# Optimization experiments

Measured on AMD Instinct MI355X. Metric: run time of the kernel, lower is better.

Reference implementation:

```python
import jax, jax.numpy as jnp
import numpy as np

C = 256


def setup_inputs() -> dict:
    key = jax.random.key(0)
    keys = jax.random.split(key, 14)
    shp = (2, C, 64, 256)
    inp = {f"x{i}": jax.random.normal(keys[i], shp, dtype=jnp.float32) for i in range(12)}
    # ConvTranspose2d weight [in, out, 1, 1] -> squeezed to [in, out]
    inp["W"] = jax.random.normal(keys[12], (C, C), dtype=jnp.float32) * 0.05
    inp["b"] = jax.random.normal(keys[13], (C,), dtype=jnp.float32) * 0.05
    return inp


def reference(x0, x1, x2, x3, x4, x5, x6, x7, x8, x9, x10, x11, W, b):
    xs = jnp.stack([x0, x1, x2, x3, x4, x5, x6, x7, x8, x9, x10, x11])  # [12,B,C,H,Wd]
    # 1x1 conv-transpose == per-pixel matmul over channels (weight is [in,out])
    y = jnp.einsum('ibchw,co->ibohw', xs, W)  # [12,B,C,H,Wd]
    n, B, Co, H, Wd = y.shape
    Hout = 12 * H
    # interleave: output row 12*h + i comes from tensor i, row h
    out = jnp.transpose(y, (1, 2, 3, 0, 4)).reshape(B, Co, Hout, Wd)
    # bias multiplicity: conv-transpose bias fills ALL rows of each (12H-11)-row
    # intermediate; padded copy j covers rows j .. j+12H-12 of the final buffer
    r = jnp.arange(Hout)
    count = (jnp.minimum(11, r) - jnp.maximum(0, r - Hout + 12) + 1).astype(out.dtype)
    out = out + b[:, None, None] * count[None, :, None]
    return out
```

## Files before the change

### kernel.cpp

```cpp
#include <hip/hip_runtime.h>


typedef __attribute__((ext_vector_type(8))) short bf16x8;
typedef __attribute__((ext_vector_type(4))) float f32x4;

#define ROW_B 512
#define TILE_B (64 * ROW_B)

struct Ptrs12 { const float* p[12]; };

__device__ __forceinline__ unsigned f2bf1(float f) {
  unsigned u = __float_as_uint(f);
  return (u + 0x7FFFu + ((u >> 16) & 1u)) >> 16;
}

__global__ void w_prepass(const float* __restrict__ W, unsigned short* __restrict__ Wf) {
  int idx = blockIdx.x * 256 + threadIdx.x;
  int j = idx & 7, l = (idx >> 3) & 63, s = (idx >> 9) & 7, u = idx >> 12;
  int c = s * 32 + (l >> 4) * 8 + j;
  int o = u * 16 + (l & 15);
  Wf[idx] = (unsigned short)f2bf1(W[c * 256 + o]);
}

__global__ __launch_bounds__(512, 2) void gemm12(Ptrs12 xs,
                                                 const unsigned short* __restrict__ Wf,
                                                 const float* __restrict__ bias,
                                                 float* __restrict__ out) {
  __shared__ char smem[2 * TILE_B];
  const int tid = threadIdx.x;
  const int v = tid >> 6;
  const int l = tid & 63;
  const int q = l >> 4;
  const int m = l & 15;

  bf16x8 wf[2][8];
#pragma unroll
  for (int tt = 0; tt < 2; ++tt)
#pragma unroll
    for (int s = 0; s < 8; ++s) {
      int u = v * 2 + tt;
      wf[tt][s] = *(const bf16x8*)(Wf + (((u * 8 + s) * 64 + l) << 3));
    }
  const float bv0 = bias[v * 32 + m];
  const float bv1 = bias[v * 32 + 16 + m];

  const int tile0 = blockIdx.x * 12;
  float4 pf[2][4];

  auto tload = [&](int tile) {
    int row = tile >> 2, w0 = (tile & 3) << 6;
    int i = row >> 7, bb = (row >> 6) & 1, h = row & 63;
    const float* xp = xs.p[i] + (size_t)bb * 4194304 + h * 256 + w0 + m * 4;
#pragma unroll
    for (int it = 0; it < 2; ++it) {
      int cb = it * 128 + v * 16 + q * 4;
#pragma unroll
      for (int dc = 0; dc < 4; ++dc)
        pf[it][dc] = *(const float4*)(xp + (size_t)(cb + dc) * 16384);
    }
  };
  auto twrite = [&](int bs) {
    char* lb = smem + bs * TILE_B;
#pragma unroll
    for (int it = 0; it < 2; ++it) {
      int cb = it * 128 + v * 16 + q * 4;
#pragma unroll
      for (int k = 0; k < 4; ++k) {
        unsigned lo = f2bf1(((const float*)&pf[it][0])[k]) |
                      (f2bf1(((const float*)&pf[it][1])[k]) << 16);
        unsigned hi = f2bf1(((const float*)&pf[it][2])[k]) |
                      (f2bf1(((const float*)&pf[it][3])[k]) << 16);
        uint2 val; val.x = lo; val.y = hi;
        *(uint2*)(lb + (m * 4 + k) * ROW_B + cb * 2) = val;
      }
    }
  };

  tload(tile0);
  twrite(0);
  __syncthreads();

#pragma unroll 1
  for (int mt = 0; mt < 12; ++mt) {
    int tile = tile0 + mt;
    if (mt < 11) tload(tile + 1);

    f32x4 acc[4][2];
#pragma unroll
    for (int a = 0; a < 4; ++a) { acc[a][0] = 0.0f; acc[a][1] = 0.0f; }

    const char* lb = smem + (mt & 1) * TILE_B;
#pragma unroll
    for (int s = 0; s < 8; ++s) {
      bf16x8 af[4];
#pragma unroll
      for (int m16 = 0; m16 < 4; ++m16)
        af[m16] = *(const bf16x8*)(lb + (m16 * 16 + m) * ROW_B + s * 64 + q * 16);
#pragma unroll
      for (int m16 = 0; m16 < 4; ++m16) {
        acc[m16][0] = __builtin_amdgcn_mfma_f32_16x16x32_bf16(af[m16], wf[0][s], acc[m16][0], 0, 0, 0);
        acc[m16][1] = __builtin_amdgcn_mfma_f32_16x16x32_bf16(af[m16], wf[1][s], acc[m16][1], 0, 0, 0);
      }
    }

    if (mt < 11) twrite((mt + 1) & 1);

    int row = tile >> 2, w0 = (tile & 3) << 6;
    int i = row >> 7, bb = (row >> 6) & 1, h = row & 63;
    int r = h * 12 + i;
    int cnt_i = (r < 11 ? r : 11) - (r > 756 ? r - 756 : 0) + 1;
    float cnt = (float)cnt_i;
    size_t ob = (size_t)bb * 50331648u + (size_t)r * 256 + w0 + q * 4;
#pragma unroll
    for (int tt = 0; tt < 2; ++tt) {
      float ba = (tt ? bv1 : bv0) * cnt;
      float* op = out + ob + (size_t)(v * 32 + tt * 16 + m) * 196608;
#pragma unroll
      for (int m16 = 0; m16 < 4; ++m16) {
        float4 sv;
        sv.x = acc[m16][tt][0] + ba;
        sv.y = acc[m16][tt][1] + ba;
        sv.z = acc[m16][tt][2] + ba;
        sv.w = acc[m16][tt][3] + ba;
        *(float4*)(op + m16 * 16) = sv;
      }
    }
    __syncthreads();
  }
}

extern "C" void kernel_launch(void* const* d_in, const int* in_sizes, int n_in,
                              void* d_out, int out_size, void* d_ws, size_t ws_size,
                              hipStream_t stream) {
  Ptrs12 xs;
  for (int i = 0; i < 12; ++i) xs.p[i] = (const float*)d_in[i];
  const float* W = (const float*)d_in[12];
  const float* bias = (const float*)d_in[13];
  unsigned short* Wf = (unsigned short*)d_ws;

  hipLaunchKernelGGL(w_prepass, dim3(256), dim3(256), 0, stream, W, Wf);
  hipLaunchKernelGGL(gemm12, dim3(512), dim3(512), 0, stream, xs, Wf, bias, (float*)d_out);
}
```

Before: 710.5 us.

## Use 1024-thread blocks with 16 output channels per wave and swizzled LDS

Result: slower. 778.2 us (+9.5%).

```diff
diff --git a/kernel.cpp b/kernel.cpp
--- a/kernel.cpp
+++ b/kernel.cpp
@@ -22,10 +22,17 @@
   Wf[idx] = (unsigned short)f2bf1(W[c * 256 + o]);
 }
 
-__global__ __launch_bounds__(512, 2) void gemm12(Ptrs12 xs,
-                                                 const unsigned short* __restrict__ Wf,
-                                                 const float* __restrict__ bias,
-                                                 float* __restrict__ out) {
+#define LBAR() do {                                   \
+  __builtin_amdgcn_sched_barrier(0);                  \
+  asm volatile("s_waitcnt lgkmcnt(0)" ::: "memory");  \
+  __builtin_amdgcn_s_barrier();                       \
+  __builtin_amdgcn_sched_barrier(0);                  \
+} while (0)
+
+__global__ __launch_bounds__(1024, 4) void gemm12(Ptrs12 xs,
+                                                  const unsigned short* __restrict__ Wf,
+                                                  const float* __restrict__ bias,
+                                                  float* __restrict__ out) {
   __shared__ char smem[2 * TILE_B];
   const int tid = threadIdx.x;
   const int v = tid >> 6;
@@ -33,99 +40,92 @@
   const int q = l >> 4;
   const int m = l & 15;
 
-  bf16x8 wf[2][8];
+  bf16x8 wf[8];
 #pragma unroll
-  for (int tt = 0; tt < 2; ++tt)
-#pragma unroll
-    for (int s = 0; s < 8; ++s) {
-      int u = v * 2 + tt;
-      wf[tt][s] = *(const bf16x8*)(Wf + (((u * 8 + s) * 64 + l) << 3));
-    }
-  const float bv0 = bias[v * 32 + m];
-  const float bv1 = bias[v * 32 + 16 + m];
+  for (int s = 0; s < 8; ++s)
+    wf[s] = *(const bf16x8*)(Wf + (((v * 8 + s) * 64 + l) << 3));
+  const float bv = bias[v * 16 + m];
 
-  const int tile0 = blockIdx.x * 12;
-  float4 pf[2][4];
+  const int tile0 = blockIdx.x * 24;
+  float4 pf[4];
 
   auto tload = [&](int tile) {
     int row = tile >> 2, w0 = (tile & 3) << 6;
     int i = row >> 7, bb = (row >> 6) & 1, h = row & 63;
     const float* xp = xs.p[i] + (size_t)bb * 4194304 + h * 256 + w0 + m * 4;
+    int cb = v * 16 + q * 4;
 #pragma unroll
-    for (int it = 0; it < 2; ++it) {
-      int cb = it * 128 + v * 16 + q * 4;
-#pragma unroll
-      for (int dc = 0; dc < 4; ++dc)
-        pf[it][dc] = *(const float4*)(xp + (size_t)(cb + dc) * 16384);
-    }
+    for (int dc = 0; dc < 4; ++dc)
+      pf[dc] = *(const float4*)(xp + (size_t)(cb + dc) * 16384);
   };
   auto twrite = [&](int bs) {
     char* lb = smem + bs * TILE_B;
+    const int col = v * 32 + q * 8;
 #pragma unroll
-    for (int it = 0; it < 2; ++it) {
-      int cb = it * 128 + v * 16 + q * 4;
-#pragma unroll
-      for (int k = 0; k < 4; ++k) {
-        unsigned lo = f2bf1(((const float*)&pf[it][0])[k]) |
-                      (f2bf1(((const float*)&pf[it][1])[k]) << 16);
-        unsigned hi = f2bf1(((const float*)&pf[it][2])[k]) |
-                      (f2bf1(((const float*)&pf[it][3])[k]) << 16);
-        uint2 val; val.x = lo; val.y = hi;
-        *(uint2*)(lb + (m * 4 + k) * ROW_B + cb * 2) = val;
-      }
+    for (int k = 0; k < 4; ++k) {
+      unsigned lo = f2bf1(((const float*)&pf[0])[k]) |
+                    (f2bf1(((const float*)&pf[1])[k]) << 16);
+      unsigned hi = f2bf1(((const float*)&pf[2])[k]) |
+                    (f2bf1(((const float*)&pf[3])[k]) << 16);
+      uint2 val; val.x = lo; val.y = hi;
+      int row = m * 4 + k;
+      unsigned a = (unsigned)(row * ROW_B + col) ^ ((unsigned)(row & 7) << 4);
+      *(uint2*)(lb + a) = val;
     }
   };
 
   tload(tile0);
   twrite(0);
-  __syncthreads();
+  LBAR();
 
 #pragma unroll 1
-  for (int mt = 0; mt < 12; ++mt) {
-    int tile = tile0 + mt;
-    if (mt < 11) tload(tile + 1);
+  for (int mt = 0; mt < 24; ++mt) {
+    const int tile = tile0 + mt;
+    if (mt < 23) tload(tile + 1);
 
-    f32x4 acc[4][2];
+    f32x4 acc[4];
 #pragma unroll
-    for (int a = 0; a < 4; ++a) { acc[a][0] = 0.0f; acc[a][1] = 0.0f; }
+    for (int z = 0; z < 4; ++z) acc[z] = 0.0f;
 
     const char* lb = smem + (mt & 1) * TILE_B;
 #pragma unroll
     for (int s = 0; s < 8; ++s) {
       bf16x8 af[4];
 #pragma unroll
+      for (int m16 = 0; m16 < 4; ++m16) {
+        int row = m16 * 16 + m;
+        unsigned a = (unsigned)(row * ROW_B + s * 64 + q * 16) ^
+                     ((unsigned)(row & 7) << 4);
+        af[m16] = *(const bf16x8*)(lb + a);
+      }
+#pragma unroll
       for (int m16 = 0; m16 < 4; ++m16)
-        af[m16] = *(const bf16x8*)(lb + (m16 * 16 + m) * ROW_B + s * 64 + q * 16);
+        acc[m16] = __builtin_amdgcn_mfma_f32_16x16x32_bf16(af[m16], wf[s], acc[m16], 0, 0, 0);
+    }
+
+    {
+      int row = tile >> 2, w0 = (tile & 3) << 6;
+      int i = row >> 7, bb = (row >> 6) & 1, h = row & 63;
+      int r = h * 12 + i;
+      int cnt_i = (r < 11 ? r : 11) - (r > 756 ? r - 756 : 0) + 1;
+      float ba = bv * (float)cnt_i;
+      float* op = out + (size_t)bb * 50331648u + (size_t)r * 256 + w0 + q * 4
+                      + (size_t)(v * 16 + m) * 196608;
 #pragma unroll
       for (int m16 = 0; m16 < 4; ++m16) {
-        acc[m16][0] = __builtin_amdgcn_mfma_f32_16x16x32_bf16(af[m16], wf[0][s], acc[m16][0], 0, 0, 0);
-        acc[m16][1] = __builtin_amdgcn_mfma_f32_16x16x32_bf16(af[m16], wf[1][s], acc[m16][1], 0, 0, 0);
+        float4 sv;
+        sv.x = acc[m16][0] + ba;
+        sv.y = acc[m16][1] + ba;
+        sv.z = acc[m16][2] + ba;
+        sv.w = acc[m16][3] + ba;
+        *(float4*)(op + m16 * 16) = sv;
       }
     }
 
-    if (mt < 11) twrite((mt + 1) & 1);
-
-    int row = tile >> 2, w0 = (tile & 3) << 6;
-    int i = row >> 7, bb = (row >> 6) & 1, h = row & 63;
-    int r = h * 12 + i;
-    int cnt_i = (r < 11 ? r : 11) - (r > 756 ? r - 756 : 0) + 1;
-    float cnt = (float)cnt_i;
-    size_t ob = (size_t)bb * 50331648u + (size_t)r * 256 + w0 + q * 4;
-#pragma unroll
-    for (int tt = 0; tt < 2; ++tt) {
-      float ba = (tt ? bv1 : bv0) * cnt;
-      float* op = out + ob + (size_t)(v * 32 + tt * 16 + m) * 196608;
-#pragma unroll
-      for (int m16 = 0; m16 < 4; ++m16) {
-        float4 sv;
-        sv.x = acc[m16][tt][0] + ba;
-        sv.y = acc[m16][tt][1] + ba;
-        sv.z = acc[m16][tt][2] + ba;
-        sv.w = acc[m16][tt][3] + ba;
-        *(float4*)(op + m16 * 16) = sv;
-      }
+    if (mt < 23) {
+      twrite((mt + 1) & 1);
+      LBAR();
     }
-    __syncthreads();
   }
 }
 
@@ -139,5 +139,5 @@
   unsigned short* Wf = (unsigned short*)d_ws;
 
   hipLaunchKernelGGL(w_prepass, dim3(256), dim3(256), 0, stream, W, Wf);
-  hipLaunchKernelGGL(gemm12, dim3(512), dim3(512), 0, stream, xs, Wf, bias, (float*)d_out);
+  hipLaunchKernelGGL(gemm12, dim3(256), dim3(1024), 0, stream, xs, Wf, bias, (float*)d_out);
 }
```

## Halve tile width, raise occupancy, swizzle LDS, and use a lighter barrier

Applied to the files above, without the earlier changes.

Result: slower. 803.9 us (+13.1%).

```diff
diff --git a/kernel.cpp b/kernel.cpp
--- a/kernel.cpp
+++ b/kernel.cpp
@@ -5,7 +5,7 @@
 typedef __attribute__((ext_vector_type(4))) float f32x4;
 
 #define ROW_B 512
-#define TILE_B (64 * ROW_B)
+#define TILE_B (32 * ROW_B)
 
 struct Ptrs12 { const float* p[12]; };
 
@@ -22,7 +22,14 @@
   Wf[idx] = (unsigned short)f2bf1(W[c * 256 + o]);
 }
 
-__global__ __launch_bounds__(512, 2) void gemm12(Ptrs12 xs,
+#define LBAR() do {                                   \
+  __builtin_amdgcn_sched_barrier(0);                  \
+  asm volatile("s_waitcnt lgkmcnt(0)" ::: "memory");  \
+  __builtin_amdgcn_s_barrier();                       \
+  __builtin_amdgcn_sched_barrier(0);                  \
+} while (0)
+
+__global__ __launch_bounds__(512, 4) void gemm12(Ptrs12 xs,
                                                  const unsigned short* __restrict__ Wf,
                                                  const float* __restrict__ bias,
                                                  float* __restrict__ out) {
@@ -44,88 +51,92 @@
   const float bv0 = bias[v * 32 + m];
   const float bv1 = bias[v * 32 + 16 + m];
 
-  const int tile0 = blockIdx.x * 12;
-  float4 pf[2][4];
+  const int wg = m & 7;
+  const int chb = v * 32 + q * 8 + ((m >> 3) << 2);
+
+  const int tile0 = blockIdx.x * 24;
+  float4 pf[4];
 
   auto tload = [&](int tile) {
-    int row = tile >> 2, w0 = (tile & 3) << 6;
+    int row = tile >> 3, w0 = (tile & 7) << 5;
     int i = row >> 7, bb = (row >> 6) & 1, h = row & 63;
-    const float* xp = xs.p[i] + (size_t)bb * 4194304 + h * 256 + w0 + m * 4;
+    const float* xp = xs.p[i] + (size_t)bb * 4194304 + h * 256 + w0 + wg * 4;
 #pragma unroll
-    for (int it = 0; it < 2; ++it) {
-      int cb = it * 128 + v * 16 + q * 4;
-#pragma unroll
-      for (int dc = 0; dc < 4; ++dc)
-        pf[it][dc] = *(const float4*)(xp + (size_t)(cb + dc) * 16384);
-    }
+    for (int dc = 0; dc < 4; ++dc)
+      pf[dc] = *(const float4*)(xp + (size_t)(chb + dc) * 16384);
   };
   auto twrite = [&](int bs) {
     char* lb = smem + bs * TILE_B;
 #pragma unroll
-    for (int it = 0; it < 2; ++it) {
-      int cb = it * 128 + v * 16 + q * 4;
-#pragma unroll
-      for (int k = 0; k < 4; ++k) {
-        unsigned lo = f2bf1(((const float*)&pf[it][0])[k]) |
-                      (f2bf1(((const float*)&pf[it][1])[k]) << 16);
-        unsigned hi = f2bf1(((const float*)&pf[it][2])[k]) |
-                      (f2bf1(((const float*)&pf[it][3])[k]) << 16);
-        uint2 val; val.x = lo; val.y = hi;
-        *(uint2*)(lb + (m * 4 + k) * ROW_B + cb * 2) = val;
-      }
+    for (int k = 0; k < 4; ++k) {
+      unsigned lo = f2bf1(((const float*)&pf[0])[k]) |
+                    (f2bf1(((const float*)&pf[1])[k]) << 16);
+      unsigned hi = f2bf1(((const float*)&pf[2])[k]) |
+                    (f2bf1(((const float*)&pf[3])[k]) << 16);
+      uint2 val; val.x = lo; val.y = hi;
+      int row = wg * 4 + k;
+      unsigned a = (unsigned)(row * ROW_B + chb * 2) ^ ((unsigned)(row & 7) << 4);
+      *(uint2*)(lb + a) = val;
     }
   };
 
   tload(tile0);
   twrite(0);
-  __syncthreads();
+  LBAR();
 
 #pragma unroll 1
-  for (int mt = 0; mt < 12; ++mt) {
-    int tile = tile0 + mt;
-    if (mt < 11) tload(tile + 1);
+  for (int mt = 0; mt < 24; ++mt) {
+    const int tile = tile0 + mt;
+    if (mt < 23) tload(tile + 1);
 
-    f32x4 acc[4][2];
+    f32x4 acc[2][2];
 #pragma unroll
-    for (int a = 0; a < 4; ++a) { acc[a][0] = 0.0f; acc[a][1] = 0.0f; }
+    for (int z = 0; z < 2; ++z) { acc[z][0] = 0.0f; acc[z][1] = 0.0f; }
 
     const char* lb = smem + (mt & 1) * TILE_B;
 #pragma unroll
     for (int s = 0; s < 8; ++s) {
-      bf16x8 af[4];
+      bf16x8 af[2];
 #pragma unroll
-      for (int m16 = 0; m16 < 4; ++m16)
-        af[m16] = *(const bf16x8*)(lb + (m16 * 16 + m) * ROW_B + s * 64 + q * 16);
+      for (int m16 = 0; m16 < 2; ++m16) {
+        int row = m16 * 16 + m;
+        unsigned a = (unsigned)(row * ROW_B + s * 64 + q * 16) ^
+                     ((unsigned)(row & 7) << 4);
+        af[m16] = *(const bf16x8*)(lb + a);
+      }
 #pragma unroll
-      for (int m16 = 0; m16 < 4; ++m16) {
+      for (int m16 = 0; m16 < 2; ++m16) {
         acc[m16][0] = __builtin_amdgcn_mfma_f32_16x16x32_bf16(af[m16], wf[0][s], acc[m16][0], 0, 0, 0);
         acc[m16][1] = __builtin_amdgcn_mfma_f32_16x16x32_bf16(af[m16], wf[1][s], acc[m16][1], 0, 0, 0);
       }
     }
 
-    if (mt < 11) twrite((mt + 1) & 1);
+    if (mt < 23) twrite((mt + 1) & 1);
 
-    int row = tile >> 2, w0 = (tile & 3) << 6;
-    int i = row >> 7, bb = (row >> 6) & 1, h = row & 63;
-    int r = h * 12 + i;
-    int cnt_i = (r < 11 ? r : 11) - (r > 756 ? r - 756 : 0) + 1;
-    float cnt = (float)cnt_i;
-    size_t ob = (size_t)bb * 50331648u + (size_t)r * 256 + w0 + q * 4;
+    {
+      int row = tile >> 3, w0 = (tile & 7) << 5;
+      int i = row >> 7, bb = (row >> 6) & 1, h = row & 63;
+      int r = h * 12 + i;
+      int cnt_i = (r < 11 ? r : 11) - (r > 756 ? r - 756 : 0) + 1;
+      float cnt = (float)cnt_i;
+      size_t ob = (size_t)bb * 50331648u + (size_t)r * 256 + w0 + q * 4;
 #pragma unroll
-    for (int tt = 0; tt < 2; ++tt) {
-      float ba = (tt ? bv1 : bv0) * cnt;
-      float* op = out + ob + (size_t)(v * 32 + tt * 16 + m) * 196608;
+      for (int tt = 0; tt < 2; ++tt) {
+        float ba = (tt ? bv1 : bv0) * cnt;
+        float* op = out + ob + (size_t)(v * 32 + tt * 16 + m) * 196608;
 #pragma unroll
-      for (int m16 = 0; m16 < 4; ++m16) {
-        float4 sv;
-        sv.x = acc[m16][tt][0] + ba;
-        sv.y = acc[m16][tt][1] + ba;
-        sv.z = acc[m16][tt][2] + ba;
-        sv.w = acc[m16][tt][3] + ba;
-        *(float4*)(op + m16 * 16) = sv;
+        for (int m16 = 0; m16 < 2; ++m16) {
+          float4 sv;
+          sv.x = acc[m16][tt][0] + ba;
+          sv.y = acc[m16][tt][1] + ba;
+          sv.z = acc[m16][tt][2] + ba;
+          sv.w = acc[m16][tt][3] + ba;
+          *(float4*)(op + m16 * 16) = sv;
+        }
       }
     }
-    __syncthreads();
+
+    if (mt < 23) LBAR();
   }
 }
 
```
